# Optimization experiments

Measured on AMD Instinct MI355X. Metric: run time of the kernel, lower is better.

## Reference

```python
import jax, jax.numpy as jnp
import numpy as np

B, S, D = 8, 2048, 256


def setup_inputs() -> dict:
    key = jax.random.key(0)
    kq, kk, kv, km = jax.random.split(key, 4)
    q = jax.random.normal(kq, (B, S, D), dtype=jnp.float32)
    k = jax.random.normal(kk, (B, S, D), dtype=jnp.float32)
    v = jax.random.normal(kv, (B, S, D), dtype=jnp.float32)
    mask = jax.random.randint(km, (B, S, S), 0, 2, dtype=jnp.int32)
    return {"q": q, "k": k, "v": v, "mask": mask}


def reference(q, k, v, mask):
    d_k = q.shape[-1]
    scale = 1.0 / jnp.sqrt(jnp.float32(d_k))
    # scores: [B, S, S]
    attn = jnp.einsum('bqd,bkd->bqk', q, k) * scale
    attn = jnp.where(mask == 0, jnp.float32(-1e9), attn)
    attn = jax.nn.softmax(attn, axis=-1)
    out = jnp.einsum('bqk,bkd->bqd', attn, v)
    return (out, attn)
```

## Files before the change

kernel.cpp:

```cpp
#include <hip/hip_runtime.h>

constexpr int B = 8, S = 2048, D = 256;
constexpr int TQ = 32;
constexpr float SCALE = 0.0625f;
constexpr int PSTRIDE = 2056;

typedef __attribute__((ext_vector_type(8))) short bf16x8;
typedef __attribute__((ext_vector_type(4))) float f32x4;

__device__ __forceinline__ short f2bf(float f) {
    union { float f; unsigned u; } c; c.f = f;
    unsigned u = c.u + 0x7fffu + ((c.u >> 16) & 1u);
    return (short)(u >> 16);
}

__global__ __launch_bounds__(256) void prepass(
    const float* __restrict__ q, const float* __restrict__ k,
    const float* __restrict__ v, const int* __restrict__ mask,
    short* __restrict__ qb, short* __restrict__ kb,
    short* __restrict__ vtb, unsigned short* __restrict__ pm)
{
    __shared__ float tile[64][65];
    const int blk = blockIdx.x;
    const int tid = threadIdx.x;

    if (blk < 8192) {
        const float* in = (blk < 4096) ? q : k;
        short* out = (blk < 4096) ? qb : kb;
        int i = (blk & 4095) * 256 + tid;
        float4 x = ((const float4*)in)[i];
        short4 o; o.x = f2bf(x.x); o.y = f2bf(x.y); o.z = f2bf(x.z); o.w = f2bf(x.w);
        ((short4*)out)[i] = o;
    } else if (blk < 9216) {
        int blk2 = blk - 8192;
        int b = blk2 >> 7, rem = blk2 & 127;
        int d0 = (rem & 3) * 64, k0 = (rem >> 2) * 64;
        int tr = tid >> 4, tc = tid & 15;
        const float* vb = v + (size_t)b * S * D;
        #pragma unroll
        for (int r = 0; r < 4; ++r) {
            int key = r * 16 + tr;
            float4 x = *(const float4*)(vb + (size_t)(k0 + key) * D + d0 + tc * 4);
            tile[key][tc * 4 + 0] = x.x; tile[key][tc * 4 + 1] = x.y;
            tile[key][tc * 4 + 2] = x.z; tile[key][tc * 4 + 3] = x.w;
        }
        __syncthreads();
        short* vtbb = vtb + (size_t)b * D * S;
        #pragma unroll
        for (int r = 0; r < 4; ++r) {
            int d = r * 16 + tr;
            short4 o;
            o.x = f2bf(tile[tc * 4 + 0][d]); o.y = f2bf(tile[tc * 4 + 1][d]);
            o.z = f2bf(tile[tc * 4 + 2][d]); o.w = f2bf(tile[tc * 4 + 3][d]);
            *(short4*)(vtbb + (size_t)(d0 + d) * S + k0 + tc * 4) = o;
        }
    } else {
        int t2 = blk - 9216;
        int w = tid >> 6, lane = tid & 63;
        int l16 = lane & 15;
        int rowlin = t2 * 4 + w;
        const int* mrow = mask + (size_t)rowlin * S;
        unsigned short* pmrow = pm + (size_t)rowlin * 128;
        #pragma unroll
        for (int g = 0; g < 8; ++g) {
            unsigned v16 = 0;
            #pragma unroll
            for (int u = 0; u < 4; ++u) {
                int col = g * 256 + u * 64 + lane;
                unsigned long long bal = __ballot(mrow[col] != 0);
                unsigned nib = (unsigned)((bal >> l16) & 1ull)
                             | (unsigned)((bal >> (l16 + 16)) & 1ull) << 1
                             | (unsigned)((bal >> (l16 + 32)) & 1ull) << 2
                             | (unsigned)((bal >> (l16 + 48)) & 1ull) << 3;
                v16 |= nib << (u * 4);
            }
            if (lane < 16) pmrow[g * 16 + l16] = (unsigned short)v16;
        }
    }
}

__global__ __launch_bounds__(512, 2) void attn_mfma(
    const short* __restrict__ qb, const short* __restrict__ kb,
    const short* __restrict__ vtb, const unsigned short* __restrict__ pmg,
    float* __restrict__ outg, float* __restrict__ attng)
{
    const int b = blockIdx.x & 7;
    const int i0 = (blockIdx.x >> 3) * TQ;
    const int tid = threadIdx.x;
    const int wave = tid >> 6, lane = tid & 63;
    const int quad = lane >> 4, l16 = lane & 15;

    __shared__ short p_lds[TQ][PSTRIDE];
    __shared__ float red[8][TQ];

    unsigned pmv[2][4];
    {
        const unsigned short* pmb = pmg + (((size_t)b * S + i0 + quad * 4) * 8 + wave) * 16 + l16;
        #pragma unroll
        for (int mt = 0; mt < 2; ++mt)
            #pragma unroll
            for (int r = 0; r < 4; ++r)
                pmv[mt][r] = pmb[(size_t)(mt * 16 + r) * 128];
    }

    bf16x8 aq[2][8];
    const short* qbase = qb + ((size_t)b * S + i0) * D;
    #pragma unroll
    for (int mt = 0; mt < 2; ++mt)
        #pragma unroll
        for (int ks = 0; ks < 8; ++ks)
            aq[mt][ks] = *(const bf16x8*)(qbase + (size_t)(mt * 16 + l16) * D + ks * 32 + quad * 8);

    f32x4 acc[2][16];
    #pragma unroll
    for (int mt = 0; mt < 2; ++mt)
        #pragma unroll
        for (int nt = 0; nt < 16; ++nt)
            acc[mt][nt] = f32x4{0.f, 0.f, 0.f, 0.f};

    const short* kbase = kb + (size_t)b * S * D;
    #pragma unroll
    for (int nt = 0; nt < 16; ++nt) {
        const int n0 = wave * 256 + nt * 16;
        bf16x8 bk[8];
        #pragma unroll
        for (int ks = 0; ks < 8; ++ks)
            bk[ks] = *(const bf16x8*)(kbase + (size_t)(n0 + l16) * D + ks * 32 + quad * 8);
        #pragma unroll
        for (int ks = 0; ks < 8; ++ks) {
            acc[0][nt] = __builtin_amdgcn_mfma_f32_16x16x32_bf16(aq[0][ks], bk[ks], acc[0][nt], 0, 0, 0);
            acc[1][nt] = __builtin_amdgcn_mfma_f32_16x16x32_bf16(aq[1][ks], bk[ks], acc[1][nt], 0, 0, 0);
        }
    }

    float rsum[2][4];
    #pragma unroll
    for (int mt = 0; mt < 2; ++mt)
        #pragma unroll
        for (int r = 0; r < 4; ++r) rsum[mt][r] = 0.f;

    #pragma unroll
    for (int mt = 0; mt < 2; ++mt) {
        #pragma unroll
        for (int nt = 0; nt < 16; ++nt) {
            #pragma unroll
            for (int r = 0; r < 4; ++r) {
                float s = acc[mt][nt][r] * SCALE;
                float sv = ((pmv[mt][r] >> nt) & 1u) ? s : -1e9f;
                float e = __expf(sv);
                acc[mt][nt][r] = e;
                rsum[mt][r] += e;
            }
        }
    }
    #pragma unroll
    for (int mt = 0; mt < 2; ++mt)
        #pragma unroll
        for (int r = 0; r < 4; ++r) {
            float v = rsum[mt][r];
            v += __shfl_xor(v, 1); v += __shfl_xor(v, 2);
            v += __shfl_xor(v, 4); v += __shfl_xor(v, 8);
            rsum[mt][r] = v;
            if (l16 == 0) red[wave][mt * 16 + quad * 4 + r] = v;
        }
    __syncthreads();

    float inv[2][4];
    #pragma unroll
    for (int mt = 0; mt < 2; ++mt)
        #pragma unroll
        for (int r = 0; r < 4; ++r) {
            float tot = 0.f;
            #pragma unroll
            for (int w = 0; w < 8; ++w) tot += red[w][mt * 16 + quad * 4 + r];
            inv[mt][r] = 1.0f / tot;
        }

    #pragma unroll
    for (int mt = 0; mt < 2; ++mt) {
        float* abase = attng + ((size_t)b * S + i0 + mt * 16 + quad * 4) * S;
        #pragma unroll
        for (int nt = 0; nt < 16; ++nt) {
            const int col = wave * 256 + nt * 16 + l16;
            #pragma unroll
            for (int r = 0; r < 4; ++r) {
                float p = acc[mt][nt][r] * inv[mt][r];
                abase[(size_t)r * S + col] = p;
                p_lds[mt * 16 + quad * 4 + r][col] = f2bf(p);
            }
        }
    }
    __syncthreads();

    f32x4 oacc[2][2];
    #pragma unroll
    for (int mt = 0; mt < 2; ++mt)
        #pragma unroll
        for (int nc = 0; nc < 2; ++nc) oacc[mt][nc] = f32x4{0.f, 0.f, 0.f, 0.f};

    const short* vbase = vtb + (size_t)b * D * S;
    const int nb = wave * 32;
    for (int ks = 0; ks < 64; ++ks) {
        bf16x8 ap[2], bv[2];
        #pragma unroll
        for (int mt = 0; mt < 2; ++mt)
            ap[mt] = *(const bf16x8*)&p_lds[mt * 16 + l16][ks * 32 + quad * 8];
        #pragma unroll
        for (int nc = 0; nc < 2; ++nc)
            bv[nc] = *(const bf16x8*)(vbase + (size_t)(nb + nc * 16 + l16) * S + ks * 32 + quad * 8);
        #pragma unroll
        for (int mt = 0; mt < 2; ++mt)
            #pragma unroll
            for (int nc = 0; nc < 2; ++nc)
                oacc[mt][nc] = __builtin_amdgcn_mfma_f32_16x16x32_bf16(ap[mt], bv[nc], oacc[mt][nc], 0, 0, 0);
    }

    #pragma unroll
    for (int mt = 0; mt < 2; ++mt)
        #pragma unroll
        for (int nc = 0; nc < 2; ++nc)
            #pragma unroll
            for (int r = 0; r < 4; ++r) {
                int row = i0 + mt * 16 + quad * 4 + r;
                int col = nb + nc * 16 + l16;
                outg[((size_t)b * S + row) * D + col] = oacc[mt][nc][r];
            }
}

extern "C" void kernel_launch(void* const* d_in, const int* in_sizes, int n_in,
                              void* d_out, int out_size, void* d_ws, size_t ws_size,
                              hipStream_t stream) {
    const float* q    = (const float*)d_in[0];
    const float* k    = (const float*)d_in[1];
    const float* v    = (const float*)d_in[2];
    const int*   mask = (const int*)d_in[3];
    float* out  = (float*)d_out;
    float* attn = out + (size_t)B * S * D;

    const size_t N = (size_t)B * S * D;
    short* qb  = (short*)d_ws;
    short* kb  = qb + N;
    short* vtb = kb + N;
    unsigned short* pm = (unsigned short*)(vtb + N);

    prepass<<<dim3(13312), 256, 0, stream>>>(q, k, v, mask, qb, kb, vtb, pm);
    attn_mfma<<<dim3((S / TQ) * B), 512, 0, stream>>>(qb, kb, vtb, pm, out, attn);
}
```

Before: 412.4 us.

## Fuse mask bit-packing and Q bf16 conversion into the attention kernel

Moves the mask-to-bitmask packing and the Q fp32-to-bf16 conversion out of the prepass and into the attention kernel. Each block ballots its own 32 mask rows into a shared-memory bitmask and converts its Q tile on load. This removes the prepass writes and re-reads of packed mask and bf16 Q. The cost is extra LDS use and a sync in a kernel that already holds a large LDS buffer, and mask loads now sit in front of the main compute, which may hurt occupancy or latency hiding.

```diff
diff --git a/kernel.cpp b/kernel.cpp
--- a/kernel.cpp
+++ b/kernel.cpp
@@ -15,24 +15,20 @@
 }
 
 __global__ __launch_bounds__(256) void prepass(
-    const float* __restrict__ q, const float* __restrict__ k,
-    const float* __restrict__ v, const int* __restrict__ mask,
-    short* __restrict__ qb, short* __restrict__ kb,
-    short* __restrict__ vtb, unsigned short* __restrict__ pm)
+    const float* __restrict__ k, const float* __restrict__ v,
+    short* __restrict__ kb, short* __restrict__ vtb)
 {
     __shared__ float tile[64][65];
     const int blk = blockIdx.x;
     const int tid = threadIdx.x;
 
-    if (blk < 8192) {
-        const float* in = (blk < 4096) ? q : k;
-        short* out = (blk < 4096) ? qb : kb;
-        int i = (blk & 4095) * 256 + tid;
-        float4 x = ((const float4*)in)[i];
+    if (blk < 4096) {
+        int i = blk * 256 + tid;
+        float4 x = ((const float4*)k)[i];
         short4 o; o.x = f2bf(x.x); o.y = f2bf(x.y); o.z = f2bf(x.z); o.w = f2bf(x.w);
-        ((short4*)out)[i] = o;
-    } else if (blk < 9216) {
-        int blk2 = blk - 8192;
+        ((short4*)kb)[i] = o;
+    } else {
+        int blk2 = blk - 4096;
         int b = blk2 >> 7, rem = blk2 & 127;
         int d0 = (rem & 3) * 64, k0 = (rem >> 2) * 64;
         int tr = tid >> 4, tc = tid & 15;
@@ -54,34 +50,12 @@
             o.z = f2bf(tile[tc * 4 + 2][d]); o.w = f2bf(tile[tc * 4 + 3][d]);
             *(short4*)(vtbb + (size_t)(d0 + d) * S + k0 + tc * 4) = o;
         }
-    } else {
-        int t2 = blk - 9216;
-        int w = tid >> 6, lane = tid & 63;
-        int l16 = lane & 15;
-        int rowlin = t2 * 4 + w;
-        const int* mrow = mask + (size_t)rowlin * S;
-        unsigned short* pmrow = pm + (size_t)rowlin * 128;
-        #pragma unroll
-        for (int g = 0; g < 8; ++g) {
-            unsigned v16 = 0;
-            #pragma unroll
-            for (int u = 0; u < 4; ++u) {
-                int col = g * 256 + u * 64 + lane;
-                unsigned long long bal = __ballot(mrow[col] != 0);
-                unsigned nib = (unsigned)((bal >> l16) & 1ull)
-                             | (unsigned)((bal >> (l16 + 16)) & 1ull) << 1
-                             | (unsigned)((bal >> (l16 + 32)) & 1ull) << 2
-                             | (unsigned)((bal >> (l16 + 48)) & 1ull) << 3;
-                v16 |= nib << (u * 4);
-            }
-            if (lane < 16) pmrow[g * 16 + l16] = (unsigned short)v16;
-        }
     }
 }
 
 __global__ __launch_bounds__(512, 2) void attn_mfma(
-    const short* __restrict__ qb, const short* __restrict__ kb,
-    const short* __restrict__ vtb, const unsigned short* __restrict__ pmg,
+    const float* __restrict__ qf, const short* __restrict__ kb,
+    const short* __restrict__ vtb, const int* __restrict__ maskg,
     float* __restrict__ outg, float* __restrict__ attng)
 {
     const int b = blockIdx.x & 7;
@@ -92,24 +66,51 @@
 
     __shared__ short p_lds[TQ][PSTRIDE];
     __shared__ float red[8][TQ];
-
-    unsigned pmv[2][4];
+    __shared__ unsigned short pm_lds[TQ][8][16];
+
     {
-        const unsigned short* pmb = pmg + (((size_t)b * S + i0 + quad * 4) * 8 + wave) * 16 + l16;
-        #pragma unroll
-        for (int mt = 0; mt < 2; ++mt)
-            #pragma unroll
-            for (int r = 0; r < 4; ++r)
-                pmv[mt][r] = pmb[(size_t)(mt * 16 + r) * 128];
-    }
+        const int* mrow_base = maskg + ((size_t)b * S + i0 + wave * 4) * S;
+        #pragma unroll 1
+        for (int rr = 0; rr < 4; ++rr) {
+            const int* mrow = mrow_base + (size_t)rr * S;
+            int mv[32];
+            #pragma unroll
+            for (int g = 0; g < 8; ++g)
+                #pragma unroll
+                for (int u = 0; u < 4; ++u)
+                    mv[g * 4 + u] = mrow[g * 256 + u * 64 + lane];
+            #pragma unroll
+            for (int g = 0; g < 8; ++g) {
+                unsigned v16 = 0;
+                #pragma unroll
+                for (int u = 0; u < 4; ++u) {
+                    unsigned long long bal = __ballot(mv[g * 4 + u] != 0);
+                    unsigned nib = (unsigned)((bal >> l16) & 1ull)
+                                 | (unsigned)((bal >> (l16 + 16)) & 1ull) << 1
+                                 | (unsigned)((bal >> (l16 + 32)) & 1ull) << 2
+                                 | (unsigned)((bal >> (l16 + 48)) & 1ull) << 3;
+                    v16 |= nib << (u * 4);
+                }
+                if (lane < 16) pm_lds[wave * 4 + rr][g][l16] = (unsigned short)v16;
+            }
+        }
+    }
+    __syncthreads();
 
     bf16x8 aq[2][8];
-    const short* qbase = qb + ((size_t)b * S + i0) * D;
-    #pragma unroll
-    for (int mt = 0; mt < 2; ++mt)
-        #pragma unroll
-        for (int ks = 0; ks < 8; ++ks)
-            aq[mt][ks] = *(const bf16x8*)(qbase + (size_t)(mt * 16 + l16) * D + ks * 32 + quad * 8);
+    const float* qbase = qf + ((size_t)b * S + i0) * D;
+    #pragma unroll
+    for (int mt = 0; mt < 2; ++mt)
+        #pragma unroll
+        for (int ks = 0; ks < 8; ++ks) {
+            const float* p = qbase + (size_t)(mt * 16 + l16) * D + ks * 32 + quad * 8;
+            float4 x0 = *(const float4*)p;
+            float4 x1 = *(const float4*)(p + 4);
+            bf16x8 a;
+            a[0] = f2bf(x0.x); a[1] = f2bf(x0.y); a[2] = f2bf(x0.z); a[3] = f2bf(x0.w);
+            a[4] = f2bf(x1.x); a[5] = f2bf(x1.y); a[6] = f2bf(x1.z); a[7] = f2bf(x1.w);
+            aq[mt][ks] = a;
+        }
 
     f32x4 acc[2][16];
     #pragma unroll
@@ -132,6 +133,13 @@
             acc[1][nt] = __builtin_amdgcn_mfma_f32_16x16x32_bf16(aq[1][ks], bk[ks], acc[1][nt], 0, 0, 0);
         }
     }
+
+    unsigned pmv[2][4];
+    #pragma unroll
+    for (int mt = 0; mt < 2; ++mt)
+        #pragma unroll
+        for (int r = 0; r < 4; ++r)
+            pmv[mt][r] = pm_lds[mt * 16 + quad * 4 + r][wave][l16];
 
     float rsum[2][4];
     #pragma unroll
@@ -238,11 +246,9 @@
     float* attn = out + (size_t)B * S * D;
 
     const size_t N = (size_t)B * S * D;
-    short* qb  = (short*)d_ws;
-    short* kb  = qb + N;
+    short* kb  = (short*)d_ws;
     short* vtb = kb + N;
-    unsigned short* pm = (unsigned short*)(vtb + N);
-
-    prepass<<<dim3(13312), 256, 0, stream>>>(q, k, v, mask, qb, kb, vtb, pm);
-    attn_mfma<<<dim3((S / TQ) * B), 512, 0, stream>>>(qb, kb, vtb, pm, out, attn);
-}
+
+    prepass<<<dim3(5120), 256, 0, stream>>>(k, v, kb, vtb);
+    attn_mfma<<<dim3((S / TQ) * B), 512, 0, stream>>>(q, kb, vtb, mask, out, attn);
+}
```

Measured after the change: 411.0 us. About the same (-0.3%).
